# Kernel tuning notes

Hardware: AMD Instinct MI355X
Metric: run time of the kernel (lower is better)

Reference implementation:

```python
import jax, jax.numpy as jnp
import numpy as np

B, T, N, C = 8, 16, 2048, 512


def setup_inputs() -> dict:
    key = jax.random.key(0)
    k1, k2, k3, k4, k5, k6 = jax.random.split(key, 6)
    return {
        "vd_s": jax.random.normal(k1, (B, T, C), dtype=jnp.float32),
        "vd_nodes": jax.random.normal(k2, (B, N, C), dtype=jnp.float32),
        # 1x1 conv weights initialized N(0, 0.01) as in the torch module
        "W1": jax.random.normal(k3, (C, C), dtype=jnp.float32) * 0.01,
        "b1": jax.random.normal(k4, (C,), dtype=jnp.float32) * 0.01,
        "W2": jax.random.normal(k5, (C, C), dtype=jnp.float32) * 0.01,
        "b2": jax.random.normal(k6, (C,), dtype=jnp.float32) * 0.01,
    }


def reference(vd_s, vd_nodes, W1, b1, W2, b2):
    # propagation_step = 1 (as in the original module)
    def per_graph(s, nodes):
        # s: [T, C] scene features, nodes: [N, C] node features
        out_scene = s.mean(axis=0)                     # [C]
        state = nodes                                  # [N, C]
        # 1x1 convs on [N, C, 1, 1] == per-node linear layers
        mat1 = state @ W1.T + b1                       # [N, C]
        mat2 = state @ W2.T + b2                       # [N, C]
        adj = mat1 @ mat2.T                            # [N, N]
        soft_adj = jax.nn.softmax(adj, axis=1)         # row-softmax (dim=1)
        new_state = soft_adj @ state + state           # message update + residual
        gp_out = new_state.mean(axis=0)                # [C]
        return jnp.concatenate([out_scene, gp_out], axis=0)  # [2C]

    return jax.vmap(per_graph)(vd_s, vd_nodes)         # [B, 2C]
```

## Files before the change

kernel.cpp:

```cpp
#include <hip/hip_runtime.h>

typedef __bf16 bf16;
typedef __bf16 bf16x8 __attribute__((ext_vector_type(8), aligned(16)));
typedef float  f32x4  __attribute__((ext_vector_type(4)));

#define B_ 8
#define T_ 16
#define N_ 2048
#define C_ 512

__device__ inline bf16x8 load8_f32(const float* p) {
    float4 a = *(const float4*)p;
    float4 b = *(const float4*)(p + 4);
    bf16x8 r;
    r[0] = (bf16)a.x; r[1] = (bf16)a.y; r[2] = (bf16)a.z; r[3] = (bf16)a.w;
    r[4] = (bf16)b.x; r[5] = (bf16)b.y; r[6] = (bf16)b.z; r[7] = (bf16)b.w;
    return r;
}

__device__ inline void gload_lds16(const bf16* g, bf16* l) {
    __builtin_amdgcn_global_load_lds(
        (const __attribute__((address_space(1))) void*)g,
        (__attribute__((address_space(3))) void*)l, 16, 0, 0);
}

__global__ __launch_bounds__(256) void k_prep(
    const float* __restrict__ vd_s, const float* __restrict__ nodes,
    const float* __restrict__ W1, const float* __restrict__ W2,
    float* __restrict__ out, bf16* __restrict__ nodes_bf,
    bf16* __restrict__ W1t, bf16* __restrict__ W2t) {
    __shared__ float sh[32 * 33];
    const int bx = blockIdx.x, tid = threadIdx.x;
    if (bx < 2048) {
        size_t i = ((size_t)bx * 256 + tid) * 16;
        *(bf16x8*)(nodes_bf + i)     = load8_f32(nodes + i);
        *(bf16x8*)(nodes_bf + i + 8) = load8_f32(nodes + i + 8);
    } else if (bx < 2064) {
        int gt = (bx - 2048) * 256 + tid;
        int b = gt >> 9, c = gt & 511;
        float s = 0.f;
#pragma unroll
        for (int t = 0; t < T_; ++t) s += vd_s[(size_t)b * T_ * C_ + t * C_ + c];
        out[b * 2 * C_ + c] = s * (1.0f / T_);
    } else {
        const float* W = (bx < 2320) ? W1 : W2;
        bf16* Wt = (bx < 2320) ? W1t : W2t;
        int idx = (bx < 2320) ? bx - 2064 : bx - 2320;
        int bxx = (idx & 15) * 32, byy = (idx >> 4) * 32;
        int tx = tid & 31, ty = tid >> 5;
#pragma unroll
        for (int r = 0; r < 32; r += 8)
            sh[(ty + r) * 33 + tx] = W[(size_t)(byy + ty + r) * C_ + bxx + tx];
        __syncthreads();
#pragma unroll
        for (int r = 0; r < 32; r += 8)
            Wt[(size_t)(bxx + ty + r) * C_ + byy + tx] = (bf16)sh[tx * 33 + ty + r];
    }
}

__global__ void k_q(const float* __restrict__ b1, const bf16* __restrict__ W2t,
                    float* __restrict__ q) {
    int wid = threadIdx.x >> 6, lane = threadIdx.x & 63;
    int c = blockIdx.x * 4 + wid;
    bf16x8 v8 = *(const bf16x8*)(W2t + (size_t)c * C_ + lane * 8);
    float s = 0.f;
#pragma unroll
    for (int i = 0; i < 8; ++i) s += (float)v8[i] * b1[lane * 8 + i];
#pragma unroll
    for (int m = 32; m; m >>= 1) s += __shfl_xor(s, m);
    if (lane == 0) q[c] = s;
}

__global__ __launch_bounds__(256) void gemm_nt(
    const bf16* __restrict__ A, size_t strideA,
    const bf16* __restrict__ Bm, size_t strideB,
    const float* __restrict__ bias,
    bf16* __restrict__ C, size_t strideC,
    int N, int K) {
    __shared__ __attribute__((aligned(16))) bf16 lA[128 * 64];
    __shared__ __attribute__((aligned(16))) bf16 lB[128 * 64];
    const int tid = threadIdx.x;
    const int lane = tid & 63, w = tid >> 6;
    const int wm = w >> 1, wn = w & 1;
    const int z = blockIdx.z;
    const int bm = blockIdx.x * 128, bn = blockIdx.y * 128;
    const bf16* Ab = A + (size_t)z * strideA;
    const bf16* Bb = Bm + (size_t)z * strideB;

    f32x4 acc[4][4];
#pragma unroll
    for (int i = 0; i < 4; ++i)
#pragma unroll
        for (int j = 0; j < 4; ++j) acc[i][j] = f32x4{0.f, 0.f, 0.f, 0.f};

    const int nkt = K >> 6;
    for (int kt = 0; kt < nkt; ++kt) {
#pragma unroll
        for (int c = 0; c < 4; ++c) {
            int ca = c * 256 + tid;
            int row = ca >> 3;
            int qd = (ca & 7) ^ (row & 7);
            gload_lds16(Ab + (size_t)(bm + row) * K + kt * 64 + qd * 8,
                        lA + c * 2048 + w * 512);
            gload_lds16(Bb + (size_t)(bn + row) * K + kt * 64 + qd * 8,
                        lB + c * 2048 + w * 512);
        }
        __syncthreads();

        bf16x8 af[2][4], bfr[2][4];
#pragma unroll
        for (int ks = 0; ks < 2; ++ks) {
            int y = ks * 4 + (lane >> 4);
#pragma unroll
            for (int i = 0; i < 4; ++i) {
                int ra = wm * 64 + i * 16 + (lane & 15);
                int rb = wn * 64 + i * 16 + (lane & 15);
                af[ks][i]  = *(const bf16x8*)&lA[ra * 64 + ((y ^ (ra & 7)) * 8)];
                bfr[ks][i] = *(const bf16x8*)&lB[rb * 64 + ((y ^ (rb & 7)) * 8)];
            }
        }
#pragma unroll
        for (int ks = 0; ks < 2; ++ks)
#pragma unroll
            for (int i = 0; i < 4; ++i)
#pragma unroll
                for (int j = 0; j < 4; ++j)
                    acc[i][j] = __builtin_amdgcn_mfma_f32_16x16x32_bf16(
                        af[ks][i], bfr[ks][j], acc[i][j], 0, 0, 0);
        __syncthreads();
    }

    bf16* Cb = C + (size_t)z * strideC;
#pragma unroll
    for (int i = 0; i < 4; ++i) {
#pragma unroll
        for (int j = 0; j < 4; ++j) {
            int col = bn + wn * 64 + j * 16 + (lane & 15);
            float bv = bias ? bias[col] : 0.f;
#pragma unroll
            for (int r = 0; r < 4; ++r) {
                int row = bm + wm * 64 + i * 16 + (lane >> 4) * 4 + r;
                Cb[(size_t)row * N + col] = (bf16)(acc[i][j][r] + bv);
            }
        }
    }
}

__global__ __launch_bounds__(512, 2) void gemm256p(
    const bf16* __restrict__ A, const bf16* __restrict__ Bm,
    bf16* __restrict__ P) {
    __shared__ __attribute__((aligned(16))) bf16 ls[2][2][16384];
    const int tid = threadIdx.x;
    const int lane = tid & 63, w = tid >> 6;
    const int wm = w >> 2, wn = w & 3;
    const int id = blockIdx.x;
    const int sw = (id & 7) * 64 + (id >> 3);
    const int z = sw >> 6, tt = sw & 63;
    const int bm = (tt >> 3) * 256, bn = (tt & 7) * 256;
    const bf16* Ab = A + (size_t)z * N_ * C_;
    const bf16* Bb = Bm + (size_t)z * N_ * C_;

    f32x4 acc[8][4];
#pragma unroll
    for (int i = 0; i < 8; ++i)
#pragma unroll
        for (int j = 0; j < 4; ++j) acc[i][j] = f32x4{0.f, 0.f, 0.f, 0.f};

#define STAGE_H(MATP, BASE, h, kt_, buf_, abi)                                    \
    {                                                                             \
        _Pragma("unroll")                                                         \
        for (int sl = 0; sl < 2; ++sl) {                                          \
            int cc = sl * 512 + tid;                                              \
            int row = (h) * 128 + (cc >> 3);                                      \
            int qd = (cc & 7) ^ (row & 7);                                        \
            gload_lds16(MATP + (size_t)((BASE) + row) * C_ + (kt_) * 64 + qd * 8, \
                        &ls[buf_][abi][((h) * 1024 + sl * 512 + w * 64) * 8]);    \
        }                                                                         \
    }
#define PH_GATE                                                         \
    __builtin_amdgcn_s_barrier();                                       \
    asm volatile("s_waitcnt lgkmcnt(0)" ::: "memory");                  \
    __builtin_amdgcn_sched_barrier(0);                                  \
    __builtin_amdgcn_s_setprio(1);

    STAGE_H(Ab, bm, 0, 0, 0, 0); STAGE_H(Ab, bm, 1, 0, 0, 0);
    STAGE_H(Bb, bn, 0, 0, 0, 1); STAGE_H(Bb, bn, 1, 0, 0, 1);
    STAGE_H(Bb, bn, 0, 1, 1, 1); STAGE_H(Bb, bn, 1, 1, 1, 1);
    asm volatile("s_waitcnt vmcnt(4)" ::: "memory");
    __builtin_amdgcn_s_barrier();

#pragma unroll
    for (int j = 0; j < 8; ++j) {
        const int cur = j & 1, nxt = cur ^ 1;
        const bf16* lA = &ls[cur][0][0];
        const bf16* lB = &ls[cur][1][0];
        bf16x8 af[4][2], b0[2][2], b1v[2][2];

#pragma unroll
        for (int i = 0; i < 4; ++i) {
            int ra = wm * 128 + i * 16 + (lane & 15);
#pragma unroll
            for (int ks = 0; ks < 2; ++ks) {
                int y = ks * 4 + (lane >> 4);
                af[i][ks] = *(const bf16x8*)&lA[ra * 64 + ((y ^ (ra & 7)) * 8)];
            }
        }
#pragma unroll
        for (int jj = 0; jj < 2; ++jj) {
            int rb = wn * 64 + jj * 16 + (lane & 15);
#pragma unroll
            for (int ks = 0; ks < 2; ++ks) {
                int y = ks * 4 + (lane >> 4);
                b0[jj][ks] = *(const bf16x8*)&lB[rb * 64 + ((y ^ (rb & 7)) * 8)];
            }
        }
        if (j < 7) STAGE_H(Ab, bm, 0, j + 1, nxt, 0);
        PH_GATE
#pragma unroll
        for (int ks = 0; ks < 2; ++ks)
#pragma unroll
            for (int i = 0; i < 4; ++i)
#pragma unroll
                for (int jj = 0; jj < 2; ++jj)
                    acc[i][jj] = __builtin_amdgcn_mfma_f32_16x16x32_bf16(
                        af[i][ks], b0[jj][ks], acc[i][jj], 0, 0, 0);
        __builtin_amdgcn_s_setprio(0);

#pragma unroll
        for (int jj = 0; jj < 2; ++jj) {
            int rb = wn * 64 + 32 + jj * 16 + (lane & 15);
#pragma unroll
            for (int ks = 0; ks < 2; ++ks) {
                int y = ks * 4 + (lane >> 4);
                b1v[jj][ks] = *(const bf16x8*)&lB[rb * 64 + ((y ^ (rb & 7)) * 8)];
            }
        }
        if (j < 7) STAGE_H(Ab, bm, 1, j + 1, nxt, 0);
        PH_GATE
#pragma unroll
        for (int ks = 0; ks < 2; ++ks)
#pragma unroll
            for (int i = 0; i < 4; ++i)
#pragma unroll
                for (int jj = 0; jj < 2; ++jj)
                    acc[i][2 + jj] = __builtin_amdgcn_mfma_f32_16x16x32_bf16(
                        af[i][ks], b1v[jj][ks], acc[i][2 + jj], 0, 0, 0);
        __builtin_amdgcn_s_setprio(0);

#pragma unroll
        for (int i = 0; i < 4; ++i) {
            int ra = wm * 128 + 64 + i * 16 + (lane & 15);
#pragma unroll
            for (int ks = 0; ks < 2; ++ks) {
                int y = ks * 4 + (lane >> 4);
                af[i][ks] = *(const bf16x8*)&lA[ra * 64 + ((y ^ (ra & 7)) * 8)];
            }
        }
        if (j < 6) STAGE_H(Bb, bn, 0, j + 2, cur, 1);
        PH_GATE
#pragma unroll
        for (int ks = 0; ks < 2; ++ks)
#pragma unroll
            for (int i = 0; i < 4; ++i)
#pragma unroll
                for (int jj = 0; jj < 2; ++jj)
                    acc[4 + i][jj] = __builtin_amdgcn_mfma_f32_16x16x32_bf16(
                        af[i][ks], b0[jj][ks], acc[4 + i][jj], 0, 0, 0);
        __builtin_amdgcn_s_setprio(0);

        if (j < 6) {
            STAGE_H(Bb, bn, 1, j + 2, cur, 1);
            asm volatile("s_waitcnt vmcnt(4)" ::: "memory");
        } else if (j == 6) {
            asm volatile("s_waitcnt vmcnt(0)" ::: "memory");
        }
        __builtin_amdgcn_s_barrier();
        __builtin_amdgcn_s_setprio(1);
#pragma unroll
        for (int ks = 0; ks < 2; ++ks)
#pragma unroll
            for (int i = 0; i < 4; ++i)
#pragma unroll
                for (int jj = 0; jj < 2; ++jj)
                    acc[4 + i][2 + jj] = __builtin_amdgcn_mfma_f32_16x16x32_bf16(
                        af[i][ks], b1v[jj][ks], acc[4 + i][2 + jj], 0, 0, 0);
        __builtin_amdgcn_s_setprio(0);
    }

    bf16* Pb = P + (size_t)z * N_ * N_;
#pragma unroll
    for (int fi = 0; fi < 8; ++fi) {
#pragma unroll
        for (int fj = 0; fj < 4; ++fj) {
            int roff = (fi >> 2) * 64 + (fi & 3) * 16;
            int coff = (fj >> 1) * 32 + (fj & 1) * 16;
            int col = bn + wn * 64 + coff + (lane & 15);
#pragma unroll
            for (int r = 0; r < 4; ++r) {
                int row = bm + wm * 128 + roff + (lane >> 4) * 4 + r;
                float v = __expf(fminf(acc[fi][fj][r], 30.f));
                Pb[(size_t)row * N_ + col] = (bf16)v;
            }
        }
    }
#undef STAGE_H
#undef PH_GATE
}

__global__ __launch_bounds__(256) void k_w2(const bf16* __restrict__ P,
                                            float* __restrict__ wpart) {
    __shared__ float rp[16 * 256];
    __shared__ float ri[16];
    const int tid = threadIdx.x;
    const int s = blockIdx.x, b = blockIdx.y;
    const bf16* Pb = P + (size_t)b * N_ * N_ + (size_t)s * 16 * N_;
    const int j0 = tid * 8;
    bf16x8 v[16];
#pragma unroll
    for (int r = 0; r < 16; ++r) {
        v[r] = *(const bf16x8*)&Pb[(size_t)r * N_ + j0];
        float t = 0.f;
#pragma unroll
        for (int e = 0; e < 8; ++e) t += (float)v[r][e];
        rp[r * 256 + tid] = t;
    }
    __syncthreads();
    {
        int row = tid >> 4, seg = tid & 15;
        float t = 0.f;
#pragma unroll
        for (int k = 0; k < 16; ++k) t += rp[row * 256 + seg + 16 * k];
#pragma unroll
        for (int m = 8; m; m >>= 1) t += __shfl_xor(t, m);
        if (seg == 0) ri[row] = 1.0f / t;
    }
    __syncthreads();
    float acc8[8] = {0.f, 0.f, 0.f, 0.f, 0.f, 0.f, 0.f, 0.f};
#pragma unroll
    for (int r = 0; r < 16; ++r) {
        float rr = ri[r];
#pragma unroll
        for (int e = 0; e < 8; ++e) acc8[e] += rr * (float)v[r][e];
    }
    float* wp = wpart + ((size_t)b * 128 + s) * (size_t)N_;
#pragma unroll
    for (int e = 0; e < 8; ++e) wp[j0 + e] = acc8[e];
}

__global__ __launch_bounds__(256) void k_gp(const bf16* __restrict__ nodes_bf,
                                            const float* __restrict__ wpart,
                                            float* __restrict__ gppart) {
    __shared__ float wred[4][64];
    __shared__ float wsh[64];
    __shared__ float gred[4][512];
    const int tid = threadIdx.x;
    const int slab = blockIdx.x, b = blockIdx.y;
    const int jj = tid & 63, sg = tid >> 6;
    float wacc = 0.f;
    for (int s = sg; s < 128; s += 4)
        wacc += wpart[((size_t)b * 128 + s) * N_ + slab * 64 + jj];
    wred[sg][jj] = wacc;
    __syncthreads();
    if (tid < 64)
        wsh[tid] = wred[0][tid] + wred[1][tid] + wred[2][tid] + wred[3][tid] + 1.0f;
    __syncthreads();
    const int j0 = slab * 64;
    const int cc = (tid & 63) * 8, jr = tid >> 6;
    const bf16* nb = nodes_bf + (size_t)b * N_ * C_;
    float acc8[8] = {0.f, 0.f, 0.f, 0.f, 0.f, 0.f, 0.f, 0.f};
    for (int j = jr; j < 64; j += 4) {
        float wj = wsh[j];
        bf16x8 nv = *(const bf16x8*)&nb[(size_t)(j0 + j) * C_ + cc];
#pragma unroll
        for (int e = 0; e < 8; ++e) acc8[e] += wj * (float)nv[e];
    }
#pragma unroll
    for (int e = 0; e < 8; ++e) gred[jr][cc + e] = acc8[e];
    __syncthreads();
    if (tid < 64) {
#pragma unroll
        for (int e = 0; e < 8; ++e) {
            int c = tid * 8 + e;
            gppart[((size_t)slab * 8 + b) * C_ + c] =
                gred[0][c] + gred[1][c] + gred[2][c] + gred[3][c];
        }
    }
}

__global__ void k_fin(const float* __restrict__ gppart, float* __restrict__ out) {
    int gt = blockIdx.x * 256 + threadIdx.x;
    int b = gt >> 9, c = gt & 511;
    float s = 0.f;
#pragma unroll
    for (int k = 0; k < 32; ++k) s += gppart[((size_t)k * 8 + b) * C_ + c];
    out[b * 2 * C_ + C_ + c] = s * (1.0f / N_);
}

extern "C" void kernel_launch(void* const* d_in, const int* in_sizes, int n_in,
                              void* d_out, int out_size, void* d_ws, size_t ws_size,
                              hipStream_t stream) {
    const float* vd_s  = (const float*)d_in[0];
    const float* nodes = (const float*)d_in[1];
    const float* W1    = (const float*)d_in[2];
    const float* b1    = (const float*)d_in[3];
    const float* W2    = (const float*)d_in[4];
    float* out = (float*)d_out;

    char* ws = (char*)d_ws;
    bf16*  nodes_bf = (bf16*)(ws);
    bf16*  H2       = (bf16*)(ws + ((size_t)16 << 20));
    float* wpart    = (float*)(ws + ((size_t)16 << 20));
    bf16*  P        = (bf16*)(ws + ((size_t)32 << 20));
    bf16*  W1t      = (bf16*)(ws + ((size_t)96 << 20));
    bf16*  W2t      = (bf16*)(ws + ((size_t)96 << 20) + (512u << 10));
    bf16*  Gt       = (bf16*)(ws + ((size_t)96 << 20) + (1024u << 10));
    char*  fbase    = ws + ((size_t)96 << 20) + (1536u << 10);
    float* q        = (float*)(fbase);
    float* gppart   = (float*)(fbase + 4096);

    k_prep<<<2576, 256, 0, stream>>>(vd_s, nodes, W1, W2,
                                     out, nodes_bf, W1t, W2t);
    k_q<<<128, 256, 0, stream>>>(b1, W2t, q);

    gemm_nt<<<dim3(4, 4, 1), 256, 0, stream>>>(
        W2t, 0, W1t, 0, nullptr, Gt, 0, C_, C_);
    gemm_nt<<<dim3(16, 4, 8), 256, 0, stream>>>(
        nodes_bf, (size_t)N_ * C_, Gt, 0, q,
        H2, (size_t)N_ * C_, C_, C_);
    gemm256p<<<512, 512, 0, stream>>>(H2, nodes_bf, P);

    k_w2<<<dim3(128, 8), 256, 0, stream>>>(P, wpart);
    k_gp<<<dim3(32, 8), 256, 0, stream>>>(nodes_bf, wpart, gppart);
    k_fin<<<16, 256, 0, stream>>>(gppart, out);
}
```

Before: 115.9 us.

## Simplify GEMM main loop to whole-tile double buffering with two barriers

Replaces the four-phase interleaved staging schedule, where A and B half-tiles were loaded between MFMA groups with per-phase barriers, with a plain double-buffered loop. Each iteration now loads all A and B fragments from LDS at once, issues all 64 MFMAs, then stages k-tile j+2 into the freed buffer behind a barrier and waits before the next iteration. This cuts the number of barriers and lgkmcnt waits per iteration, but holds more fragment registers live and overlaps global loads with compute less finely.

```diff
diff --git a/kernel.cpp b/kernel.cpp
--- a/kernel.cpp
+++ b/kernel.cpp
@@ -177,27 +177,27 @@
                         &ls[buf_][abi][((h) * 1024 + sl * 512 + w * 64) * 8]);    \
         }                                                                         \
     }
-#define PH_GATE                                                         \
-    __builtin_amdgcn_s_barrier();                                       \
-    asm volatile("s_waitcnt lgkmcnt(0)" ::: "memory");                  \
-    __builtin_amdgcn_sched_barrier(0);                                  \
-    __builtin_amdgcn_s_setprio(1);
-
-    STAGE_H(Ab, bm, 0, 0, 0, 0); STAGE_H(Ab, bm, 1, 0, 0, 0);
-    STAGE_H(Bb, bn, 0, 0, 0, 1); STAGE_H(Bb, bn, 1, 0, 0, 1);
-    STAGE_H(Bb, bn, 0, 1, 1, 1); STAGE_H(Bb, bn, 1, 1, 1, 1);
-    asm volatile("s_waitcnt vmcnt(4)" ::: "memory");
+#define STAGE_T(kt_, buf_)                                                        \
+    {                                                                             \
+        STAGE_H(Ab, bm, 0, kt_, buf_, 0); STAGE_H(Ab, bm, 1, kt_, buf_, 0);       \
+        STAGE_H(Bb, bn, 0, kt_, buf_, 1); STAGE_H(Bb, bn, 1, kt_, buf_, 1);       \
+    }
+
+    STAGE_T(0, 0);
+    STAGE_T(1, 1);
+    asm volatile("s_waitcnt vmcnt(8)" ::: "memory");
     __builtin_amdgcn_s_barrier();
+    asm volatile("" ::: "memory");
 
 #pragma unroll
     for (int j = 0; j < 8; ++j) {
-        const int cur = j & 1, nxt = cur ^ 1;
+        const int cur = j & 1;
         const bf16* lA = &ls[cur][0][0];
         const bf16* lB = &ls[cur][1][0];
-        bf16x8 af[4][2], b0[2][2], b1v[2][2];
-
-#pragma unroll
-        for (int i = 0; i < 4; ++i) {
+
+        bf16x8 af[8][2], bfv[4][2];
+#pragma unroll
+        for (int i = 0; i < 8; ++i) {
             int ra = wm * 128 + i * 16 + (lane & 15);
 #pragma unroll
             for (int ks = 0; ks < 2; ++ks) {
@@ -206,85 +206,36 @@
             }
         }
 #pragma unroll
-        for (int jj = 0; jj < 2; ++jj) {
+        for (int jj = 0; jj < 4; ++jj) {
             int rb = wn * 64 + jj * 16 + (lane & 15);
 #pragma unroll
             for (int ks = 0; ks < 2; ++ks) {
                 int y = ks * 4 + (lane >> 4);
-                b0[jj][ks] = *(const bf16x8*)&lB[rb * 64 + ((y ^ (rb & 7)) * 8)];
-            }
-        }
-        if (j < 7) STAGE_H(Ab, bm, 0, j + 1, nxt, 0);
-        PH_GATE
+                bfv[jj][ks] = *(const bf16x8*)&lB[rb * 64 + ((y ^ (rb & 7)) * 8)];
+            }
+        }
+        __builtin_amdgcn_s_setprio(1);
 #pragma unroll
         for (int ks = 0; ks < 2; ++ks)
 #pragma unroll
-            for (int i = 0; i < 4; ++i)
-#pragma unroll
-                for (int jj = 0; jj < 2; ++jj)
+            for (int i = 0; i < 8; ++i)
+#pragma unroll
+                for (int jj = 0; jj < 4; ++jj)
                     acc[i][jj] = __builtin_amdgcn_mfma_f32_16x16x32_bf16(
-                        af[i][ks], b0[jj][ks], acc[i][jj], 0, 0, 0);
+                        af[i][ks], bfv[jj][ks], acc[i][jj], 0, 0, 0);
         __builtin_amdgcn_s_setprio(0);
 
-#pragma unroll
-        for (int jj = 0; jj < 2; ++jj) {
-            int rb = wn * 64 + 32 + jj * 16 + (lane & 15);
-#pragma unroll
-            for (int ks = 0; ks < 2; ++ks) {
-                int y = ks * 4 + (lane >> 4);
-                b1v[jj][ks] = *(const bf16x8*)&lB[rb * 64 + ((y ^ (rb & 7)) * 8)];
-            }
-        }
-        if (j < 7) STAGE_H(Ab, bm, 1, j + 1, nxt, 0);
-        PH_GATE
-#pragma unroll
-        for (int ks = 0; ks < 2; ++ks)
-#pragma unroll
-            for (int i = 0; i < 4; ++i)
-#pragma unroll
-                for (int jj = 0; jj < 2; ++jj)
-                    acc[i][2 + jj] = __builtin_amdgcn_mfma_f32_16x16x32_bf16(
-                        af[i][ks], b1v[jj][ks], acc[i][2 + jj], 0, 0, 0);
-        __builtin_amdgcn_s_setprio(0);
-
-#pragma unroll
-        for (int i = 0; i < 4; ++i) {
-            int ra = wm * 128 + 64 + i * 16 + (lane & 15);
-#pragma unroll
-            for (int ks = 0; ks < 2; ++ks) {
-                int y = ks * 4 + (lane >> 4);
-                af[i][ks] = *(const bf16x8*)&lA[ra * 64 + ((y ^ (ra & 7)) * 8)];
-            }
-        }
-        if (j < 6) STAGE_H(Bb, bn, 0, j + 2, cur, 1);
-        PH_GATE
-#pragma unroll
-        for (int ks = 0; ks < 2; ++ks)
-#pragma unroll
-            for (int i = 0; i < 4; ++i)
-#pragma unroll
-                for (int jj = 0; jj < 2; ++jj)
-                    acc[4 + i][jj] = __builtin_amdgcn_mfma_f32_16x16x32_bf16(
-                        af[i][ks], b0[jj][ks], acc[4 + i][jj], 0, 0, 0);
-        __builtin_amdgcn_s_setprio(0);
-
-        if (j < 6) {
-            STAGE_H(Bb, bn, 1, j + 2, cur, 1);
-            asm volatile("s_waitcnt vmcnt(4)" ::: "memory");
-        } else if (j == 6) {
-            asm volatile("s_waitcnt vmcnt(0)" ::: "memory");
-        }
+        asm volatile("" ::: "memory");
         __builtin_amdgcn_s_barrier();
-        __builtin_amdgcn_s_setprio(1);
-#pragma unroll
-        for (int ks = 0; ks < 2; ++ks)
-#pragma unroll
-            for (int i = 0; i < 4; ++i)
-#pragma unroll
-                for (int jj = 0; jj < 2; ++jj)
-                    acc[4 + i][2 + jj] = __builtin_amdgcn_mfma_f32_16x16x32_bf16(
-                        af[i][ks], b1v[jj][ks], acc[4 + i][2 + jj], 0, 0, 0);
-        __builtin_amdgcn_s_setprio(0);
+        asm volatile("" ::: "memory");
+
+        if (j + 2 < 8) STAGE_T(j + 2, cur);
+        if (j < 7) {
+            if (j < 6) asm volatile("s_waitcnt vmcnt(8)" ::: "memory");
+            else       asm volatile("s_waitcnt vmcnt(0)" ::: "memory");
+            __builtin_amdgcn_s_barrier();
+            asm volatile("" ::: "memory");
+        }
     }
 
     bf16* Pb = P + (size_t)z * N_ * N_;
@@ -304,7 +255,7 @@
         }
     }
 #undef STAGE_H
-#undef PH_GATE
+#undef STAGE_T
 }
 
 __global__ __launch_bounds__(256) void k_w2(const bf16* __restrict__ P,
```

Result: slower. 130.2 us (+12.4%).
